# Optimization experiments

Measured on AMD Instinct MI355X. Metric: run time of the kernel, lower is better.

The kernel has to match this reference:

```python
import jax, jax.numpy as jnp
import numpy as np
import math

IN_F, OUT_F, RANK, ALPHA = 4096, 4096, 16, 32
SCALING = ALPHA / RANK


def setup_inputs() -> dict:
    key = jax.random.key(0)
    k_x, k_w, k_a = jax.random.split(key, 3)
    x = jax.random.normal(k_x, (4, 2048, IN_F), dtype=jnp.float32)
    weight = jax.random.normal(k_w, (OUT_F, IN_F), dtype=jnp.float32)
    bias = jnp.zeros((OUT_F,), dtype=jnp.float32)
    lora_A = jax.random.normal(k_a, (RANK, IN_F), dtype=jnp.float32) * math.sqrt(2.0 / RANK)
    lora_B = jnp.zeros((OUT_F, RANK), dtype=jnp.float32)
    return {"x": x, "weight": weight, "bias": bias, "lora_A": lora_A, "lora_B": lora_B}


def reference(x, weight, bias, lora_A, lora_B):
    # base: x @ W^T + b    [B,S,out]
    base = jnp.einsum("bsi,oi->bso", x, weight) + bias
    # faithful to source: materialize full rank-update matrix (B @ A) [out,in]
    delta_w = lora_B @ lora_A
    lora = jnp.einsum("bsi,oi->bso", x, delta_w) * SCALING
    return base + lora
```

## Files before the change

kernel.cpp:

```cpp
#include <hip/hip_runtime.h>
#include <hip/hip_bf16.h>

#define IN_F   4096
#define OUT_F  4096
#define M_ROWS 8192
#define RANK   16
#define SCALING 2.0f

#define BM 256
#define BN 256
#define BK 64
#define NT (IN_F / BK)

typedef __attribute__((ext_vector_type(8))) short bf16x8;
typedef __attribute__((ext_vector_type(4))) float f32x4;
typedef unsigned short ushort_t;

__device__ __forceinline__ short f2b(float f) {
    union { float f; unsigned u; } c; c.f = f;
    unsigned r = (c.u + 0x7FFFu + ((c.u >> 16) & 1u)) >> 16;
    return (short)r;
}

__device__ __forceinline__ float4 ld4(const float* p) { return *(const float4*)p; }

__device__ __forceinline__ float4 s4(float4 v, float s) {
    v.x *= s; v.y *= s; v.z *= s; v.w *= s; return v;
}

__device__ __forceinline__ bf16x8 pack8(float4 a, float4 b) {
    bf16x8 r;
    r[0] = f2b(a.x); r[1] = f2b(a.y); r[2] = f2b(a.z); r[3] = f2b(a.w);
    r[4] = f2b(b.x); r[5] = f2b(b.y); r[6] = f2b(b.z); r[7] = f2b(b.w);
    return r;
}

__device__ __forceinline__ void gload16(const void* g, void* l) {
    __builtin_amdgcn_global_load_lds(
        (const __attribute__((address_space(1))) unsigned int*)g,
        (__attribute__((address_space(3))) unsigned int*)l, 16, 0, 0);
}

__global__ __launch_bounds__(256) void cvt_bf16_kernel(const float* __restrict__ in,
                                                       ushort_t* __restrict__ out, int n8) {
    int i = blockIdx.x * blockDim.x + threadIdx.x;
    const int stride = gridDim.x * blockDim.x;
    for (; i < n8; i += stride) {
        const float* p = in + (size_t)i * 8;
        *(bf16x8*)(out + (size_t)i * 8) = pack8(ld4(p), ld4(p + 4));
    }
}

__global__ __launch_bounds__(256) void lora_t_mfma(const ushort_t* __restrict__ xb,
                                                   const ushort_t* __restrict__ ab,
                                                   float* __restrict__ T) {
    const int t = threadIdx.x, lane = t & 63, wv = t >> 6;
    const int r0 = blockIdx.x * 64 + wv * 16;
    const int l15 = lane & 15, lk = lane >> 4;
    const ushort_t* xr = xb + (size_t)(r0 + l15) * IN_F + lk * 8;
    const ushort_t* ar = ab + (size_t)l15 * IN_F + lk * 8;
    f32x4 acc = (f32x4){0.f, 0.f, 0.f, 0.f};
    for (int k0 = 0; k0 < IN_F; k0 += 32) {
        bf16x8 af = *(const bf16x8*)(xr + k0);
        bf16x8 bf = *(const bf16x8*)(ar + k0);
        acc = __builtin_amdgcn_mfma_f32_16x16x32_bf16(af, bf, acc, 0, 0, 0);
    }
#pragma unroll
    for (int v = 0; v < 4; v++)
        T[(size_t)(r0 + lk * 4 + v) * RANK + l15] = acc[v];
}

__global__ __launch_bounds__(512, 1) void gemm8p(
        const ushort_t* __restrict__ xb, const ushort_t* __restrict__ wb,
        const float* __restrict__ bias, const float* __restrict__ lora_B,
        const float* __restrict__ T, float* __restrict__ out) {

    __shared__ __align__(16) ushort_t As[2][BM * BK];
    __shared__ __align__(16) ushort_t Bs[2][BN * BK];

    const int tid  = threadIdx.x;
    const int lane = tid & 63, wv = tid >> 6;
    const int wm = wv >> 2, wn = wv & 3;
    const int l15 = lane & 15, lk = lane >> 4;

    const int bid = blockIdx.x;
    const int swz = (bid & 7) * 64 + (bid >> 3);
    const int by = swz >> 4, bx = swz & 15;
    const int brow = by * BM, bcol = bx * BN;

    const int off0 = wv * 2048 + lane * 16;
    const int off1 = off0 + 1024;
    const int row0 = off0 >> 7, row1 = off1 >> 7;
    const int sc0 = ((off0 & 127) ^ ((row0 & 7) << 4)) >> 1;
    const int sc1 = ((off1 & 127) ^ ((row1 & 7) << 4)) >> 1;
    const int ldst = wv * 1024;

#define STAGE_A(h, kt, bf) do { \
    gload16(xb + (size_t)(brow + (h)*128 + row0) * IN_F + (kt)*64 + sc0, &As[bf][(h)*8192 + ldst]); \
    gload16(xb + (size_t)(brow + (h)*128 + row1) * IN_F + (kt)*64 + sc1, &As[bf][(h)*8192 + ldst + 512]); \
  } while (0)
#define STAGE_B(h, kt, bf) do { \
    gload16(wb + (size_t)(bcol + (h)*128 + row0) * IN_F + (kt)*64 + sc0, &Bs[bf][(h)*8192 + ldst]); \
    gload16(wb + (size_t)(bcol + (h)*128 + row1) * IN_F + (kt)*64 + sc1, &Bs[bf][(h)*8192 + ldst + 512]); \
  } while (0)

    const int cb0 = (lk * 16) ^ ((l15 & 7) << 4);
    const int cb1 = (64 + lk * 16) ^ ((l15 & 7) << 4);

#define AFR(bf, r, cb) (*(const bf16x8*)((const char*)&As[bf][0] + (r) * 128 + (cb)))
#define BFR(bf, c, cb) (*(const bf16x8*)((const char*)&Bs[bf][0] + (c) * 128 + (cb)))

    f32x4 acc[8][4];
#pragma unroll
    for (int m = 0; m < 8; m++)
#pragma unroll
        for (int n = 0; n < 4; n++) acc[m][n] = (f32x4){0.f, 0.f, 0.f, 0.f};

    bf16x8 af[8], bf0[4], bf1[4];

    STAGE_A(0, 0, 0); STAGE_A(1, 0, 0);
    STAGE_B(0, 0, 0); STAGE_B(1, 0, 0);
    STAGE_B(0, 1, 1); STAGE_A(0, 1, 1);
    asm volatile("s_waitcnt vmcnt(4)" ::: "memory");
    __builtin_amdgcn_s_barrier();

    for (int t = 0; t < NT; ++t) {
        const int cur = t & 1, nxt = cur ^ 1;
        const int kt1 = (t + 1 < NT) ? t + 1 : NT - 1;
        const int kt2 = (t + 2 < NT) ? t + 2 : NT - 1;
        const int am = wm * 128, bn = wn * 64;

#pragma unroll
        for (int mi = 0; mi < 4; mi++) {
            af[mi * 2]     = AFR(cur, am + mi * 16 + l15, cb0);
            af[mi * 2 + 1] = AFR(cur, am + mi * 16 + l15, cb1);
        }
#pragma unroll
        for (int ni = 0; ni < 2; ni++) {
            bf0[ni * 2]     = BFR(cur, bn + ni * 16 + l15, cb0);
            bf0[ni * 2 + 1] = BFR(cur, bn + ni * 16 + l15, cb1);
        }
        STAGE_B(1, kt1, nxt);
        asm volatile("" ::: "memory");
        __builtin_amdgcn_s_barrier();
        __builtin_amdgcn_sched_barrier(0);
        __builtin_amdgcn_s_setprio(1);
#pragma unroll
        for (int mi = 0; mi < 4; mi++)
#pragma unroll
            for (int ni = 0; ni < 2; ni++)
#pragma unroll
                for (int ks = 0; ks < 2; ks++)
                    acc[mi][ni] = __builtin_amdgcn_mfma_f32_16x16x32_bf16(
                        af[mi * 2 + ks], bf0[ni * 2 + ks], acc[mi][ni], 0, 0, 0);
        __builtin_amdgcn_s_setprio(0);
        asm volatile("" ::: "memory");
        __builtin_amdgcn_s_barrier();

#pragma unroll
        for (int ni = 0; ni < 2; ni++) {
            bf1[ni * 2]     = BFR(cur, bn + 32 + ni * 16 + l15, cb0);
            bf1[ni * 2 + 1] = BFR(cur, bn + 32 + ni * 16 + l15, cb1);
        }
        STAGE_A(1, kt1, nxt);
        asm volatile("" ::: "memory");
        __builtin_amdgcn_s_barrier();
        __builtin_amdgcn_sched_barrier(0);
        __builtin_amdgcn_s_setprio(1);
#pragma unroll
        for (int mi = 0; mi < 4; mi++)
#pragma unroll
            for (int ni = 0; ni < 2; ni++)
#pragma unroll
                for (int ks = 0; ks < 2; ks++)
                    acc[mi][2 + ni] = __builtin_amdgcn_mfma_f32_16x16x32_bf16(
                        af[mi * 2 + ks], bf1[ni * 2 + ks], acc[mi][2 + ni], 0, 0, 0);
        __builtin_amdgcn_s_setprio(0);
        asm volatile("" ::: "memory");
        __builtin_amdgcn_s_barrier();

#pragma unroll
        for (int mi = 0; mi < 4; mi++) {
            af[mi * 2]     = AFR(cur, am + 64 + mi * 16 + l15, cb0);
            af[mi * 2 + 1] = AFR(cur, am + 64 + mi * 16 + l15, cb1);
        }
        STAGE_B(0, kt2, cur);
        asm volatile("" ::: "memory");
        __builtin_amdgcn_s_barrier();
        __builtin_amdgcn_sched_barrier(0);
        __builtin_amdgcn_s_setprio(1);
#pragma unroll
        for (int mi = 0; mi < 4; mi++)
#pragma unroll
            for (int ni = 0; ni < 2; ni++)
#pragma unroll
                for (int ks = 0; ks < 2; ks++)
                    acc[4 + mi][2 + ni] = __builtin_amdgcn_mfma_f32_16x16x32_bf16(
                        af[mi * 2 + ks], bf1[ni * 2 + ks], acc[4 + mi][2 + ni], 0, 0, 0);
        __builtin_amdgcn_s_setprio(0);
        asm volatile("" ::: "memory");
        __builtin_amdgcn_s_barrier();

        STAGE_A(0, kt2, cur);
        asm volatile("" ::: "memory");
        __builtin_amdgcn_s_barrier();
        __builtin_amdgcn_sched_barrier(0);
        __builtin_amdgcn_s_setprio(1);
#pragma unroll
        for (int mi = 0; mi < 4; mi++)
#pragma unroll
            for (int ni = 0; ni < 2; ni++)
#pragma unroll
                for (int ks = 0; ks < 2; ks++)
                    acc[4 + mi][ni] = __builtin_amdgcn_mfma_f32_16x16x32_bf16(
                        af[mi * 2 + ks], bf0[ni * 2 + ks], acc[4 + mi][ni], 0, 0, 0);
        __builtin_amdgcn_s_setprio(0);
        asm volatile("s_waitcnt vmcnt(4)" ::: "memory");
        __builtin_amdgcn_s_barrier();
    }

    asm volatile("s_waitcnt vmcnt(0)" ::: "memory");
    __builtin_amdgcn_s_barrier();
    {
        const int r = tid >> 1, hh = tid & 1;
        ushort_t* LA = &As[0][0];
        ushort_t* LB = &Bs[0][0];
        if (hh == 0) {
            const float* tp = T + (size_t)(brow + r) * RANK;
            *(bf16x8*)&LA[r * 32]     = pack8(s4(ld4(tp), SCALING), s4(ld4(tp + 4), SCALING));
            *(bf16x8*)&LA[r * 32 + 8] = pack8(s4(ld4(tp + 8), SCALING), s4(ld4(tp + 12), SCALING));
            const float* bp = lora_B + (size_t)(bcol + r) * RANK;
            *(bf16x8*)&LB[r * 32]     = pack8(ld4(bp), ld4(bp + 4));
            *(bf16x8*)&LB[r * 32 + 8] = pack8(ld4(bp + 8), ld4(bp + 12));
        } else {
            bf16x8 z;
#pragma unroll
            for (int i = 0; i < 8; i++) z[i] = 0;
            *(bf16x8*)&LA[r * 32 + 16] = z; *(bf16x8*)&LA[r * 32 + 24] = z;
            *(bf16x8*)&LB[r * 32 + 16] = z; *(bf16x8*)&LB[r * 32 + 24] = z;
        }
    }
    __syncthreads();
    {
        const ushort_t* LA = &As[0][0];
        const ushort_t* LB = &Bs[0][0];
        bf16x8 bfL[4];
#pragma unroll
        for (int n = 0; n < 4; n++)
            bfL[n] = *(const bf16x8*)&LB[(wn * 64 + n * 16 + l15) * 32 + lk * 8];
#pragma unroll
        for (int m = 0; m < 8; m++) {
            bf16x8 afL = *(const bf16x8*)&LA[(wm * 128 + m * 16 + l15) * 32 + lk * 8];
#pragma unroll
            for (int n = 0; n < 4; n++)
                acc[m][n] = __builtin_amdgcn_mfma_f32_16x16x32_bf16(afL, bfL[n], acc[m][n], 0, 0, 0);
        }
    }

#pragma unroll
    for (int n = 0; n < 4; n++) {
        const int col = bcol + wn * 64 + n * 16 + l15;
        const float bv = bias[col];
#pragma unroll
        for (int m = 0; m < 8; m++) {
            const int row0_ = brow + wm * 128 + m * 16 + lk * 4;
#pragma unroll
            for (int v = 0; v < 4; v++)
                out[(size_t)(row0_ + v) * OUT_F + col] = acc[m][n][v] + bv;
        }
    }
#undef STAGE_A
#undef STAGE_B
#undef AFR
#undef BFR
}

__global__ __launch_bounds__(256) void lora_t_kernel(const float* __restrict__ x,
                                                     const float* __restrict__ lora_A,
                                                     float* __restrict__ T) {
    const int t   = threadIdx.x;
    const int row = blockIdx.x * 16 + (t >> 4);
    const int rr  = t & 15;
    const float* xr = x + (size_t)row * IN_F;
    const float* ar = lora_A + (size_t)rr * IN_F;
    float acc = 0.f;
#pragma unroll 8
    for (int k = 0; k < IN_F; k += 4) {
        float4 xv = ld4(xr + k);
        float4 av = ld4(ar + k);
        acc += xv.x * av.x + xv.y * av.y + xv.z * av.z + xv.w * av.w;
    }
    T[row * RANK + rr] = acc;
}

__global__ __launch_bounds__(256) void lora_gemm_kernel(
        const float* __restrict__ x, const float* __restrict__ w,
        const float* __restrict__ bias, const float* __restrict__ lora_B,
        const float* __restrict__ T, float* __restrict__ out) {

    __shared__ __align__(16) short As[128][32];
    __shared__ __align__(16) short Bs[128][32];

    const int t    = threadIdx.x;
    const int brow = blockIdx.y * 128;
    const int bcol = blockIdx.x * 128;
    const int srow  = t >> 1;
    const int shalf = (t & 1) << 4;
    const float* xa = x + (size_t)(brow + srow) * IN_F + shalf;
    const float* wb = w + (size_t)(bcol + srow) * IN_F + shalf;
    const int lane = t & 63;
    const int wv   = t >> 6;
    const int wr   = wv >> 1, wc = wv & 1;
    const int l15  = lane & 15, lk = lane >> 4;

    f32x4 acc[4][4];
#pragma unroll
    for (int m = 0; m < 4; m++)
#pragma unroll
        for (int n = 0; n < 4; n++)
            acc[m][n] = (f32x4){0.f, 0.f, 0.f, 0.f};

    for (int k0 = 0; k0 < IN_F; k0 += 32) {
        float4 a0 = ld4(xa + k0);      float4 a1 = ld4(xa + k0 + 4);
        float4 a2 = ld4(xa + k0 + 8);  float4 a3 = ld4(xa + k0 + 12);
        float4 b0 = ld4(wb + k0);      float4 b1 = ld4(wb + k0 + 4);
        float4 b2 = ld4(wb + k0 + 8);  float4 b3 = ld4(wb + k0 + 12);

        __syncthreads();
        *(bf16x8*)&As[srow][shalf]     = pack8(a0, a1);
        *(bf16x8*)&As[srow][shalf + 8] = pack8(a2, a3);
        *(bf16x8*)&Bs[srow][shalf]     = pack8(b0, b1);
        *(bf16x8*)&Bs[srow][shalf + 8] = pack8(b2, b3);
        __syncthreads();

        bf16x8 af[4], bf[4];
#pragma unroll
        for (int m = 0; m < 4; m++) af[m] = *(bf16x8*)&As[wr * 64 + m * 16 + l15][lk * 8];
#pragma unroll
        for (int n = 0; n < 4; n++) bf[n] = *(bf16x8*)&Bs[wc * 64 + n * 16 + l15][lk * 8];
#pragma unroll
        for (int m = 0; m < 4; m++)
#pragma unroll
            for (int n = 0; n < 4; n++)
                acc[m][n] = __builtin_amdgcn_mfma_f32_16x16x32_bf16(af[m], bf[n], acc[m][n], 0, 0, 0);
    }

    __syncthreads();
    if (shalf == 0) {
        const float* tp = T + (size_t)(brow + srow) * RANK;
        *(bf16x8*)&As[srow][0] = pack8(s4(ld4(tp), SCALING), s4(ld4(tp + 4), SCALING));
        *(bf16x8*)&As[srow][8] = pack8(s4(ld4(tp + 8), SCALING), s4(ld4(tp + 12), SCALING));
        const float* bp = lora_B + (size_t)(bcol + srow) * RANK;
        *(bf16x8*)&Bs[srow][0] = pack8(ld4(bp), ld4(bp + 4));
        *(bf16x8*)&Bs[srow][8] = pack8(ld4(bp + 8), ld4(bp + 12));
    } else {
        bf16x8 z;
#pragma unroll
        for (int i = 0; i < 8; i++) z[i] = 0;
        *(bf16x8*)&As[srow][16] = z; *(bf16x8*)&As[srow][24] = z;
        *(bf16x8*)&Bs[srow][16] = z; *(bf16x8*)&Bs[srow][24] = z;
    }
    __syncthreads();
    {
        bf16x8 af[4], bf[4];
#pragma unroll
        for (int m = 0; m < 4; m++) af[m] = *(bf16x8*)&As[wr * 64 + m * 16 + l15][lk * 8];
#pragma unroll
        for (int n = 0; n < 4; n++) bf[n] = *(bf16x8*)&Bs[wc * 64 + n * 16 + l15][lk * 8];
#pragma unroll
        for (int m = 0; m < 4; m++)
#pragma unroll
            for (int n = 0; n < 4; n++)
                acc[m][n] = __builtin_amdgcn_mfma_f32_16x16x32_bf16(af[m], bf[n], acc[m][n], 0, 0, 0);
    }

    const int ocol0 = bcol + wc * 64 + l15;
#pragma unroll
    for (int n = 0; n < 4; n++) {
        const int col = ocol0 + n * 16;
        const float bv = bias[col];
#pragma unroll
        for (int m = 0; m < 4; m++) {
            const int row0 = brow + wr * 64 + m * 16 + lk * 4;
#pragma unroll
            for (int v = 0; v < 4; v++) {
                out[(size_t)(row0 + v) * OUT_F + col] = acc[m][n][v] + bv;
            }
        }
    }
}

extern "C" void kernel_launch(void* const* d_in, const int* in_sizes, int n_in,
                              void* d_out, int out_size, void* d_ws, size_t ws_size,
                              hipStream_t stream) {
    const float* x      = (const float*)d_in[0];
    const float* w      = (const float*)d_in[1];
    const float* bias   = (const float*)d_in[2];
    const float* lora_A = (const float*)d_in[3];
    const float* lora_B = (const float*)d_in[4];
    float* out = (float*)d_out;

    const size_t OFF_T = 0;
    const size_t OFF_A = 524288;
    const size_t OFF_W = 655360;
    const size_t OFF_X = 34209792;
    const size_t WS_NEED = 101318656;

    if (ws_size >= WS_NEED) {
        char* ws = (char*)d_ws;
        float*    T  = (float*)(ws + OFF_T);
        ushort_t* ab = (ushort_t*)(ws + OFF_A);
        ushort_t* wbp = (ushort_t*)(ws + OFF_W);
        ushort_t* xbp = (ushort_t*)(ws + OFF_X);

        cvt_bf16_kernel<<<2048, 256, 0, stream>>>(x, xbp, M_ROWS * IN_F / 8);
        cvt_bf16_kernel<<<1024, 256, 0, stream>>>(w, wbp, OUT_F * IN_F / 8);
        cvt_bf16_kernel<<<32,   256, 0, stream>>>(lora_A, ab, RANK * IN_F / 8);

        lora_t_mfma<<<M_ROWS / 64, 256, 0, stream>>>(xbp, ab, T);

        gemm8p<<<(M_ROWS / BM) * (OUT_F / BN), 512, 0, stream>>>(xbp, wbp, bias, lora_B, T, out);
    } else {
        float* T = (float*)d_ws;
        lora_t_kernel<<<M_ROWS / 16, 256, 0, stream>>>(x, lora_A, T);
        dim3 grid(OUT_F / 128, M_ROWS / 128);
        lora_gemm_kernel<<<grid, 128 * 2, 0, stream>>>(x, w, bias, lora_B, T, out);
    }
}
```

Measured before the change: 357.6 us.

## Merge three bf16 conversion launches and restructure GEMM prefetch schedule

Replaces the three separate fp32-to-bf16 conversion launches with one kernel that walks x, W and lora_A in a single grid, removing two launches and their tail effects. Inside the GEMM main loop, all four B fragments are loaded from LDS up front into one register array instead of two batches. The global-to-LDS staging order is reshuffled so that more loads are in flight, with waitcnt thresholds changed from vmcnt(4) to vmcnt(6) plus an explicit lgkmcnt wait. This raises register pressure and depends on the new wait counts being correct for the new load order.

```diff
diff --git a/kernel.cpp b/kernel.cpp
--- a/kernel.cpp
+++ b/kernel.cpp
@@ -41,13 +41,25 @@
         (__attribute__((address_space(3))) unsigned int*)l, 16, 0, 0);
 }
 
-__global__ __launch_bounds__(256) void cvt_bf16_kernel(const float* __restrict__ in,
-                                                       ushort_t* __restrict__ out, int n8) {
+__global__ __launch_bounds__(256) void cvt3_kernel(const float* __restrict__ x,
+                                                   const float* __restrict__ w,
+                                                   const float* __restrict__ a,
+                                                   ushort_t* __restrict__ xb,
+                                                   ushort_t* __restrict__ wb,
+                                                   ushort_t* __restrict__ ab) {
+    const int n8x = M_ROWS * IN_F / 8;
+    const int n8w = OUT_F * IN_F / 8;
+    const int n8a = RANK * IN_F / 8;
+    const int ntot = n8x + n8w + n8a;
     int i = blockIdx.x * blockDim.x + threadIdx.x;
     const int stride = gridDim.x * blockDim.x;
-    for (; i < n8; i += stride) {
-        const float* p = in + (size_t)i * 8;
-        *(bf16x8*)(out + (size_t)i * 8) = pack8(ld4(p), ld4(p + 4));
+    for (; i < ntot; i += stride) {
+        const float* src; ushort_t* dst; int j;
+        if (i < n8x)            { src = x; dst = xb; j = i; }
+        else if (i < n8x + n8w) { src = w; dst = wb; j = i - n8x; }
+        else                    { src = a; dst = ab; j = i - n8x - n8w; }
+        const float* p = src + (size_t)j * 8;
+        *(bf16x8*)(dst + (size_t)j * 8) = pack8(ld4(p), ld4(p + 4));
     }
 }
 
@@ -116,12 +128,11 @@
 #pragma unroll
         for (int n = 0; n < 4; n++) acc[m][n] = (f32x4){0.f, 0.f, 0.f, 0.f};
 
-    bf16x8 af[8], bf0[4], bf1[4];
-
-    STAGE_A(0, 0, 0); STAGE_A(1, 0, 0);
-    STAGE_B(0, 0, 0); STAGE_B(1, 0, 0);
-    STAGE_B(0, 1, 1); STAGE_A(0, 1, 1);
-    asm volatile("s_waitcnt vmcnt(4)" ::: "memory");
+    bf16x8 af[8], bfq[8];
+
+    STAGE_B(0, 0, 0); STAGE_B(1, 0, 0); STAGE_A(0, 0, 0); STAGE_A(1, 0, 0);
+    STAGE_B(0, 1, 1); STAGE_B(1, 1, 1); STAGE_A(0, 1, 1);
+    asm volatile("s_waitcnt vmcnt(6)" ::: "memory");
     __builtin_amdgcn_s_barrier();
 
     for (int t = 0; t < NT; ++t) {
@@ -136,12 +147,12 @@
             af[mi * 2 + 1] = AFR(cur, am + mi * 16 + l15, cb1);
         }
 #pragma unroll
-        for (int ni = 0; ni < 2; ni++) {
-            bf0[ni * 2]     = BFR(cur, bn + ni * 16 + l15, cb0);
-            bf0[ni * 2 + 1] = BFR(cur, bn + ni * 16 + l15, cb1);
-        }
-        STAGE_B(1, kt1, nxt);
-        asm volatile("" ::: "memory");
+        for (int ni = 0; ni < 4; ni++) {
+            bfq[ni * 2]     = BFR(cur, bn + ni * 16 + l15, cb0);
+            bfq[ni * 2 + 1] = BFR(cur, bn + ni * 16 + l15, cb1);
+        }
+        STAGE_A(1, kt1, nxt);
+        asm volatile("s_waitcnt lgkmcnt(8)" ::: "memory");
         __builtin_amdgcn_s_barrier();
         __builtin_amdgcn_sched_barrier(0);
         __builtin_amdgcn_s_setprio(1);
@@ -152,17 +163,12 @@
 #pragma unroll
                 for (int ks = 0; ks < 2; ks++)
                     acc[mi][ni] = __builtin_amdgcn_mfma_f32_16x16x32_bf16(
-                        af[mi * 2 + ks], bf0[ni * 2 + ks], acc[mi][ni], 0, 0, 0);
+                        af[mi * 2 + ks], bfq[ni * 2 + ks], acc[mi][ni], 0, 0, 0);
         __builtin_amdgcn_s_setprio(0);
         asm volatile("" ::: "memory");
         __builtin_amdgcn_s_barrier();
 
-#pragma unroll
-        for (int ni = 0; ni < 2; ni++) {
-            bf1[ni * 2]     = BFR(cur, bn + 32 + ni * 16 + l15, cb0);
-            bf1[ni * 2 + 1] = BFR(cur, bn + 32 + ni * 16 + l15, cb1);
-        }
-        STAGE_A(1, kt1, nxt);
+        STAGE_B(0, kt2, cur);
         asm volatile("" ::: "memory");
         __builtin_amdgcn_s_barrier();
         __builtin_amdgcn_sched_barrier(0);
@@ -174,7 +180,7 @@
 #pragma unroll
                 for (int ks = 0; ks < 2; ks++)
                     acc[mi][2 + ni] = __builtin_amdgcn_mfma_f32_16x16x32_bf16(
-                        af[mi * 2 + ks], bf1[ni * 2 + ks], acc[mi][2 + ni], 0, 0, 0);
+                        af[mi * 2 + ks], bfq[(2 + ni) * 2 + ks], acc[mi][2 + ni], 0, 0, 0);
         __builtin_amdgcn_s_setprio(0);
         asm volatile("" ::: "memory");
         __builtin_amdgcn_s_barrier();
@@ -184,7 +190,7 @@
             af[mi * 2]     = AFR(cur, am + 64 + mi * 16 + l15, cb0);
             af[mi * 2 + 1] = AFR(cur, am + 64 + mi * 16 + l15, cb1);
         }
-        STAGE_B(0, kt2, cur);
+        STAGE_B(1, kt2, cur);
         asm volatile("" ::: "memory");
         __builtin_amdgcn_s_barrier();
         __builtin_amdgcn_sched_barrier(0);
@@ -196,7 +202,7 @@
 #pragma unroll
                 for (int ks = 0; ks < 2; ks++)
                     acc[4 + mi][2 + ni] = __builtin_amdgcn_mfma_f32_16x16x32_bf16(
-                        af[mi * 2 + ks], bf1[ni * 2 + ks], acc[4 + mi][2 + ni], 0, 0, 0);
+                        af[mi * 2 + ks], bfq[(2 + ni) * 2 + ks], acc[4 + mi][2 + ni], 0, 0, 0);
         __builtin_amdgcn_s_setprio(0);
         asm volatile("" ::: "memory");
         __builtin_amdgcn_s_barrier();
@@ -213,9 +219,9 @@
 #pragma unroll
                 for (int ks = 0; ks < 2; ks++)
                     acc[4 + mi][ni] = __builtin_amdgcn_mfma_f32_16x16x32_bf16(
-                        af[mi * 2 + ks], bf0[ni * 2 + ks], acc[4 + mi][ni], 0, 0, 0);
+                        af[mi * 2 + ks], bfq[ni * 2 + ks], acc[4 + mi][ni], 0, 0, 0);
         __builtin_amdgcn_s_setprio(0);
-        asm volatile("s_waitcnt vmcnt(4)" ::: "memory");
+        asm volatile("s_waitcnt vmcnt(6)" ::: "memory");
         __builtin_amdgcn_s_barrier();
     }
 
@@ -408,22 +414,18 @@
 
     if (ws_size >= WS_NEED) {
         char* ws = (char*)d_ws;
-        float*    T  = (float*)(ws + OFF_T);
-        ushort_t* ab = (ushort_t*)(ws + OFF_A);
+        float*    T   = (float*)(ws + OFF_T);
+        ushort_t* ab  = (ushort_t*)(ws + OFF_A);
         ushort_t* wbp = (ushort_t*)(ws + OFF_W);
         ushort_t* xbp = (ushort_t*)(ws + OFF_X);
 
-        cvt_bf16_kernel<<<2048, 256, 0, stream>>>(x, xbp, M_ROWS * IN_F / 8);
-        cvt_bf16_kernel<<<1024, 256, 0, stream>>>(w, wbp, OUT_F * IN_F / 8);
-        cvt_bf16_kernel<<<32,   256, 0, stream>>>(lora_A, ab, RANK * IN_F / 8);
-
+        cvt3_kernel<<<3072, 256, 0, stream>>>(x, w, lora_A, xbp, wbp, ab);
         lora_t_mfma<<<M_ROWS / 64, 256, 0, stream>>>(xbp, ab, T);
-
         gemm8p<<<(M_ROWS / BM) * (OUT_F / BN), 512, 0, stream>>>(xbp, wbp, bias, lora_B, T, out);
     } else {
         float* T = (float*)d_ws;
         lora_t_kernel<<<M_ROWS / 16, 256, 0, stream>>>(x, lora_A, T);
         dim3 grid(OUT_F / 128, M_ROWS / 128);
-        lora_gemm_kernel<<<grid, 128 * 2, 0, stream>>>(x, w, bias, lora_B, T, out);
-    }
-}
+        lora_gemm_kernel<<<grid, 256, 0, stream>>>(x, w, bias, lora_B, T, out);
+    }
+}
```

New measurement: 362.2 us. Within noise of the previous version (+1.3%).
